# Kernel optimization log

Measured on AMD Instinct MI355X. Metric: run time of the kernel, lower is better.

Reference implementation:

```python
import math
import jax, jax.numpy as jnp
import numpy as np

HEADS = 16
REL_WINDOW = 128


def setup_inputs() -> dict:
    key = jax.random.key(0)
    k1, k2, k3, k4, k5 = jax.random.split(key, 5)
    b, s, d = 2, 2048, 1024
    hd = d // HEADS          # 64
    R = 2 * REL_WINDOW + 1   # 257
    return {
        "x": jax.random.normal(k1, (b, s, d), dtype=jnp.float32),
        "Wqkv": jax.random.normal(k2, (3 * d, d), dtype=jnp.float32) * (1.0 / math.sqrt(d)),
        "bqkv": jax.random.normal(k3, (3 * d,), dtype=jnp.float32) * 0.02,
        "Wr": jax.random.normal(k4, (R, hd), dtype=jnp.float32) * (1.0 / math.sqrt(hd)),
        "br": jax.random.normal(k5, (R,), dtype=jnp.float32) * 0.02,
    }


def reference(x, Wqkv, bqkv, Wr, br):
    b, s, d = x.shape
    h = HEADS
    hd = d // h
    w = REL_WINDOW
    scale = math.sqrt(d / h)

    # qkv projection; torch view(b,s,h,3*hd) then chunk(3, dim=-1)
    qkv = (x @ Wqkv.T + bqkv).reshape(b, s, h, 3 * hd)
    q, k, v = jnp.split(qkv, 3, axis=-1)          # each [b,s,h,hd]
    q = q.transpose(0, 2, 1, 3)                   # [b,h,s,hd]
    k = k.transpose(0, 2, 1, 3)
    v = v.transpose(0, 2, 1, 3)

    # content scores
    content = jnp.einsum('bhik,bhjk->bhij', q, k) / scale  # [b,h,s,s]

    # relative position scores: project queries to R logits, gather per (i,j) offset
    idx = jnp.arange(s)
    offsets = jnp.clip(idx[None, :] - idx[:, None], -w, w) + w  # [s,s] in [0, 2w]
    rp = jnp.einsum('bhik,rk->bhir', q, Wr) + br               # [b,h,s,R]
    pos = jnp.take_along_axis(rp, jnp.broadcast_to(offsets, (b, h, s, s)), axis=-1)

    attn = jax.nn.softmax(content + pos, axis=-1)
    out = jnp.einsum('bhij,bhjk->bhik', attn, v)  # [b,h,s,hd]
    return out.transpose(0, 2, 1, 3).reshape(b, s, d)
```

## Files before the change

kernel.cpp:

```cpp
#include <hip/hip_runtime.h>

typedef short bfrag __attribute__((ext_vector_type(8)));
typedef float f32x4 __attribute__((ext_vector_type(4)));

#define MFMA16(a, b, c) __builtin_amdgcn_mfma_f32_16x16x32_bf16((a), (b), (c), 0, 0, 0)

#define SEQ   2048
#define DMOD  1024
#define NHEAD 16
#define HDIM  64
#define RSZ   257
#define RSTRIDE 260
#define RPADN 272
#define XN    (4096*1024)
#define WN    (3072*1024)
#define LOG2E 1.44269504f

__device__ __forceinline__ unsigned short f2bf(float f) {
  unsigned int u = __float_as_uint(f);
  u += 0x7FFFu + ((u >> 16) & 1u);
  return (unsigned short)(u >> 16);
}
__device__ __forceinline__ float bf2f(unsigned short u) {
  return __uint_as_float(((unsigned int)u) << 16);
}
__device__ __forceinline__ unsigned int pkbf(float a, float b) {
#if defined(__gfx950__)
  unsigned int r;
  asm("v_cvt_pk_bf16_f32 %0, %1, %2" : "=v"(r) : "v"(a), "v"(b));
  return r;
#else
  return (unsigned int)f2bf(a) | ((unsigned int)f2bf(b) << 16);
#endif
}
__device__ __forceinline__ float fexp2(float x) {
#if __has_builtin(__builtin_amdgcn_exp2f)
  return __builtin_amdgcn_exp2f(x);
#else
  return __expf(x * 0.69314718f);
#endif
}
__device__ __forceinline__ void gl2lds16(const void* g, void* l) {
  __builtin_amdgcn_global_load_lds(
      (__attribute__((address_space(1))) void*)(g),
      (__attribute__((address_space(3))) void*)(l), 16, 0, 0);
}

__global__ __launch_bounds__(256) void cast_all(const float* __restrict__ x,
                                                const float* __restrict__ Wqkv,
                                                const float* __restrict__ Wr,
                                                unsigned short* __restrict__ xb,
                                                unsigned short* __restrict__ wb,
                                                unsigned short* __restrict__ wrb) {
  int i = (blockIdx.x * 256 + threadIdx.x) * 4;
  if (i < XN) {
    float4 v = *(const float4*)(x + i);
    ushort4 o; o.x = f2bf(v.x); o.y = f2bf(v.y); o.z = f2bf(v.z); o.w = f2bf(v.w);
    *(ushort4*)(xb + i) = o;
  } else if (i < XN + WN) {
    int j = i - XN;
    float4 v = *(const float4*)(Wqkv + j);
    ushort4 o; o.x = f2bf(v.x); o.y = f2bf(v.y); o.z = f2bf(v.z); o.w = f2bf(v.w);
    *(ushort4*)(wb + j) = o;
  } else {
    int j = i - XN - WN;
    ushort4 o;
    unsigned short t[4];
#pragma unroll
    for (int k = 0; k < 4; ++k)
      t[k] = (j + k < RSZ * HDIM) ? f2bf(Wr[j + k]) : (unsigned short)0;
    o.x = t[0]; o.y = t[1]; o.z = t[2]; o.w = t[3];
    *(ushort4*)(wrb + j) = o;
  }
}

__global__ __launch_bounds__(512) void qkv_gemm(const unsigned short* __restrict__ xb,
                                                const unsigned short* __restrict__ wb,
                                                const float* __restrict__ bqkv,
                                                unsigned short* __restrict__ qb,
                                                unsigned short* __restrict__ kbuf,
                                                unsigned short* __restrict__ vtb) {
  __shared__ unsigned short SMEM[16384];
  unsigned short* Vtmp = SMEM;
  const int tid = threadIdx.x;
  const int orig = blockIdx.x;
  const int gx = orig & 7;
  const int idx = orig >> 3;
  const int myp = gx * 4 + (idx & 3);
  const int nxp = idx >> 2;
  const int m0 = myp * 128, n0 = nxp * 128;
  const int wave = tid >> 6, lane = tid & 63;
  const int q4 = lane >> 4, l16 = lane & 15;
  const int wm = (wave & 1) * 64;
  const int wn = (wave >> 1) * 32;
  const int sw3 = l16 & 3;

  f32x4 acc[4][2];
#pragma unroll
  for (int rt = 0; rt < 4; ++rt)
#pragma unroll
    for (int ct = 0; ct < 2; ++ct) acc[rt][ct] = (f32x4){0.f, 0.f, 0.f, 0.f};

  auto STAGE = [&](int k0, int buf) {
    unsigned short* As = SMEM + buf * 8192;
    unsigned short* Bs = As + 4096;
    int r = tid >> 2, cl = (tid & 3) ^ ((tid >> 2) & 3);
    gl2lds16(xb + (size_t)(m0 + r) * DMOD + k0 + cl * 8, As + tid * 8);
    gl2lds16(wb + (size_t)(n0 + r) * DMOD + k0 + cl * 8, Bs + tid * 8);
  };

  STAGE(0, 0);
  __syncthreads();

#pragma unroll 2
  for (int jt = 0; jt < 32; ++jt) {
    const int buf = jt & 1;
    unsigned short* As = SMEM + buf * 8192;
    unsigned short* Bs = As + 4096;

    if (jt < 31) STAGE((jt + 1) * 32, buf ^ 1);

    bfrag af[4], bf[2];
#pragma unroll
    for (int rt = 0; rt < 4; ++rt)
      af[rt] = *(const bfrag*)(As + (wm + rt * 16 + l16) * 32 + ((q4 ^ sw3) * 8));
#pragma unroll
    for (int ct = 0; ct < 2; ++ct)
      bf[ct] = *(const bfrag*)(Bs + (wn + ct * 16 + l16) * 32 + ((q4 ^ sw3) * 8));
#pragma unroll
    for (int rt = 0; rt < 4; ++rt)
#pragma unroll
      for (int ct = 0; ct < 2; ++ct)
        acc[rt][ct] = MFMA16(bf[ct], af[rt], acc[rt][ct]);

    __syncthreads();
  }

  const int batch = m0 >> 11;
  const int sbase = m0 & 2047;
  const int r3 = nxp % 3;
  const bool hasV = (r3 != 0);
  const int nv0 = n0 + ((r3 == 2) ? 64 : 0);

#pragma unroll
  for (int ct = 0; ct < 2; ++ct) {
    int ng = n0 + wn + ct * 16 + q4 * 4;
    int hh = ng / 192;
    int rem = ng - hh * 192;
    int t = rem >> 6, dd = rem & 63;
    float4 b4 = *(const float4*)(bqkv + ng);
    if (t < 2) {
      unsigned short* dst = (t == 0) ? qb : kbuf;
      size_t rowo = ((size_t)(batch * NHEAD + hh)) * SEQ + sbase;
#pragma unroll
      for (int rt = 0; rt < 4; ++rt) {
        int m = wm + rt * 16 + l16;
        uint2 pv;
        pv.x = pkbf(acc[rt][ct][0] + b4.x, acc[rt][ct][1] + b4.y);
        pv.y = pkbf(acc[rt][ct][2] + b4.z, acc[rt][ct][3] + b4.w);
        *(uint2*)(dst + (rowo + m) * HDIM + dd) = pv;
      }
    } else {
#pragma unroll
      for (int rt = 0; rt < 4; ++rt) {
        int m = wm + rt * 16 + l16;
        Vtmp[(dd + 0) * 136 + m] = f2bf(acc[rt][ct][0] + b4.x);
        Vtmp[(dd + 1) * 136 + m] = f2bf(acc[rt][ct][1] + b4.y);
        Vtmp[(dd + 2) * 136 + m] = f2bf(acc[rt][ct][2] + b4.z);
        Vtmp[(dd + 3) * 136 + m] = f2bf(acc[rt][ct][3] + b4.w);
      }
    }
  }

  if (hasV) {
    __syncthreads();
    const int hh = nv0 / 192;
    unsigned short* vdst = vtb + ((size_t)(batch * NHEAD + hh)) * HDIM * SEQ;
#pragma unroll
    for (int it = 0; it < 2; ++it) {
      int u = it * 512 + tid;
      int dd = u >> 4, mc = u & 15;
      bfrag val = *(const bfrag*)(Vtmp + dd * 136 + mc * 8);
      *(bfrag*)(vdst + (size_t)dd * SEQ + sbase + mc * 8) = val;
    }
  }
}

__global__ __launch_bounds__(512) void flash_attn(const unsigned short* __restrict__ qb,
                                                  const unsigned short* __restrict__ kbuf,
                                                  const unsigned short* __restrict__ vtb,
                                                  const unsigned short* __restrict__ wrb,
                                                  const float* __restrict__ br,
                                                  unsigned short* __restrict__ rp16,
                                                  float* __restrict__ out) {
  __shared__ unsigned short SMEM[24576];
  unsigned short* WrS = SMEM;
  unsigned short* Ps  = SMEM + 16384;

  const int tid = threadIdx.x;
  const int orig = blockIdx.x;
  const int slot = orig >> 3;
  const int bh = (orig & 7) * 4 + (slot >> 4);
  const int i0 = (slot & 15) << 7;
  const int wave = tid >> 6, lane = tid & 63;
  const int q4 = lane >> 4, l16 = lane & 15;
  const int sw = l16 & 7;
  const float SC = 0.125f * LOG2E;

  const int rloc = wave * 16 + l16;
  const int ig = i0 + rloc;
  const int iw0 = i0 + wave * 16;
  const unsigned short* qrow = qb + ((size_t)bh * SEQ + ig) * HDIM;
  bfrag qf0 = *(const bfrag*)(qrow + q4 * 8);
  bfrag qf1 = *(const bfrag*)(qrow + 32 + q4 * 8);

  unsigned short* rpbase = rp16 + ((size_t)bh * SEQ + ig) * RSTRIDE;

  {
    for (int i = tid; i < RPADN * HDIM / 8; i += 512) {
      int r = i >> 3, c = i & 7;
      *(uint4*)(&WrS[r * 64 + ((c ^ (r & 7)) << 3)]) = *(const uint4*)(&wrb[i * 8]);
    }
    __syncthreads();

    const float br256 = br[256];
#pragma unroll 4
    for (int ct = 0; ct < 16; ++ct) {
      f32x4 acc = (f32x4){0.f, 0.f, 0.f, 0.f};
      bfrag w0 = *(const bfrag*)(WrS + (ct * 16 + l16) * 64 + (q4 ^ sw) * 8);
      bfrag w1 = *(const bfrag*)(WrS + (ct * 16 + l16) * 64 + ((4 + q4) ^ sw) * 8);
      acc = MFMA16(w0, qf0, acc);
      acc = MFMA16(w1, qf1, acc);
      int r = ct * 16 + q4 * 4;
      float4 b4 = *(const float4*)(br + r);
      uint2 pv;
      pv.x = pkbf((acc[0] + b4.x) * LOG2E, (acc[1] + b4.y) * LOG2E);
      pv.y = pkbf((acc[2] + b4.z) * LOG2E, (acc[3] + b4.w) * LOG2E);
      *(uint2*)(rpbase + r) = pv;
    }
    {
      f32x4 acc = (f32x4){0.f, 0.f, 0.f, 0.f};
      bfrag w0 = *(const bfrag*)(WrS + (256 + l16) * 64 + (q4 ^ sw) * 8);
      bfrag w1 = *(const bfrag*)(WrS + (256 + l16) * 64 + ((4 + q4) ^ sw) * 8);
      acc = MFMA16(w0, qf0, acc);
      acc = MFMA16(w1, qf1, acc);
      if (q4 == 0)
        rpbase[256] = f2bf((acc[0] + br256) * LOG2E);
    }
    asm volatile("s_waitcnt vmcnt(0)" ::: "memory");
    __syncthreads();
  }

  const float rpL = bf2f(rpbase[0]);
  const float rpR = bf2f(rpbase[256]);

  float m_s = -3.0e38f, l_s = 0.f;
  f32x4 oacc[4];
#pragma unroll
  for (int ct = 0; ct < 4; ++ct) oacc[ct] = (f32x4){0.f, 0.f, 0.f, 0.f};

  const unsigned short* kbase = kbuf + (size_t)bh * SEQ * HDIM;
  const unsigned short* vbase = vtb + (size_t)bh * HDIM * SEQ;

  const int sr = tid >> 3, scl = (tid & 7) ^ ((tid >> 3) & 7);

  gl2lds16(kbase + (size_t)sr * HDIM + scl * 8, SMEM + tid * 8);
  gl2lds16(vbase + (size_t)sr * SEQ + 0 + scl * 8, SMEM + 8192 + tid * 8);
  __syncthreads();

#pragma unroll 2
  for (int jt = 0; jt < 32; ++jt) {
    const int cur = jt & 1;
    const int j0 = jt * 64;
    unsigned short* Kc = SMEM + cur * 4096;
    unsigned short* Vc = SMEM + 8192 + cur * 4096;

    if (jt < 31) {
      gl2lds16(kbase + (size_t)(j0 + 64 + sr) * HDIM + scl * 8,
               SMEM + (cur ^ 1) * 4096 + tid * 8);
      gl2lds16(vbase + (size_t)sr * SEQ + (j0 + 64) + scl * 8,
               SMEM + 8192 + (cur ^ 1) * 4096 + tid * 8);
    }

    f32x4 sacc[4];
#pragma unroll
    for (int ct = 0; ct < 4; ++ct) {
      sacc[ct] = (f32x4){0.f, 0.f, 0.f, 0.f};
      bfrag k0f = *(const bfrag*)(Kc + (ct * 16 + l16) * 64 + (q4 ^ sw) * 8);
      bfrag k1f = *(const bfrag*)(Kc + (ct * 16 + l16) * 64 + ((4 + q4) ^ sw) * 8);
      sacc[ct] = MFMA16(k0f, qf0, sacc[ct]);
      sacc[ct] = MFMA16(k1f, qf1, sacc[ct]);
    }

    float p[4][4];
    const int djw = j0 - iw0;
    if (djw >= 143) {
#pragma unroll
      for (int ct = 0; ct < 4; ++ct)
#pragma unroll
        for (int reg = 0; reg < 4; ++reg)
          p[ct][reg] = sacc[ct][reg] * SC + rpR;
    } else if (djw <= -191) {
#pragma unroll
      for (int ct = 0; ct < 4; ++ct)
#pragma unroll
        for (int reg = 0; reg < 4; ++reg)
          p[ct][reg] = sacc[ct][reg] * SC + rpL;
    } else {
#pragma unroll
      for (int ct = 0; ct < 4; ++ct) {
#pragma unroll
        for (int reg = 0; reg < 4; ++reg) {
          int j = j0 + ct * 16 + q4 * 4 + reg;
          int off = j - ig;
          off = (off < -128) ? -128 : (off > 128 ? 128 : off);
          p[ct][reg] = sacc[ct][reg] * SC + bf2f(rpbase[off + 128]);
        }
      }
    }

    float mm;
    {
      float a0 = fmaxf(fmaxf(p[0][0], p[0][1]), fmaxf(p[0][2], p[0][3]));
      float a1 = fmaxf(fmaxf(p[1][0], p[1][1]), fmaxf(p[1][2], p[1][3]));
      float a2 = fmaxf(fmaxf(p[2][0], p[2][1]), fmaxf(p[2][2], p[2][3]));
      float a3 = fmaxf(fmaxf(p[3][0], p[3][1]), fmaxf(p[3][2], p[3][3]));
      mm = fmaxf(fmaxf(a0, a1), fmaxf(a2, a3));
      mm = fmaxf(mm, __shfl_xor(mm, 16));
      mm = fmaxf(mm, __shfl_xor(mm, 32));
    }
    if (!__all(mm <= m_s + 8.0f)) {
      const float mnew = fmaxf(m_s, mm);
      const float alpha = fexp2(m_s - mnew);
      m_s = mnew;
      l_s *= alpha;
#pragma unroll
      for (int ct = 0; ct < 4; ++ct)
#pragma unroll
        for (int reg = 0; reg < 4; ++reg)
          oacc[ct][reg] *= alpha;
    }
#pragma unroll
    for (int ct = 0; ct < 4; ++ct)
#pragma unroll
      for (int reg = 0; reg < 4; ++reg)
        p[ct][reg] = fexp2(p[ct][reg] - m_s);
    {
      float s0 = (p[0][0] + p[0][1]) + (p[0][2] + p[0][3]);
      float s1 = (p[1][0] + p[1][1]) + (p[1][2] + p[1][3]);
      float s2 = (p[2][0] + p[2][1]) + (p[2][2] + p[2][3]);
      float s3 = (p[3][0] + p[3][1]) + (p[3][2] + p[3][3]);
      float rs = (s0 + s1) + (s2 + s3);
      rs += __shfl_xor(rs, 16);
      rs += __shfl_xor(rs, 32);
      l_s += rs;
    }

    unsigned int* Pw = (unsigned int*)Ps;
#pragma unroll
    for (int ct = 0; ct < 4; ++ct) {
      unsigned int pk01 = pkbf(p[ct][0], p[ct][1]);
      unsigned int pk23 = pkbf(p[ct][2], p[ct][3]);
      int chunk = ct * 2 + (q4 >> 1);
      unsigned int a = rloc * 32 + ((chunk ^ sw) << 2) + ((q4 & 1) << 1);
      Pw[a] = pk01;
      Pw[a + 1] = pk23;
    }

    bfrag pf0 = *(const bfrag*)(Ps + rloc * 64 + (q4 ^ sw) * 8);
    bfrag pf1 = *(const bfrag*)(Ps + rloc * 64 + ((4 + q4) ^ sw) * 8);
#pragma unroll
    for (int ct = 0; ct < 4; ++ct) {
      bfrag v0f = *(const bfrag*)(Vc + (ct * 16 + l16) * 64 + (q4 ^ sw) * 8);
      bfrag v1f = *(const bfrag*)(Vc + (ct * 16 + l16) * 64 + ((4 + q4) ^ sw) * 8);
      oacc[ct] = MFMA16(v0f, pf0, oacc[ct]);
      oacc[ct] = MFMA16(v1f, pf1, oacc[ct]);
    }

    __syncthreads();
  }

  const int bidx = bh >> 4, hh = bh & 15;
  const float inv = 1.0f / l_s;
  float* orow = out + ((size_t)bidx * SEQ + ig) * DMOD + hh * HDIM;
#pragma unroll
  for (int ct = 0; ct < 4; ++ct) {
    float4 v;
    v.x = oacc[ct][0] * inv;
    v.y = oacc[ct][1] * inv;
    v.z = oacc[ct][2] * inv;
    v.w = oacc[ct][3] * inv;
    *(float4*)(orow + ct * 16 + q4 * 4) = v;
  }
}

extern "C" void kernel_launch(void* const* d_in, const int* in_sizes, int n_in,
                              void* d_out, int out_size, void* d_ws, size_t ws_size,
                              hipStream_t stream) {
  const float* x    = (const float*)d_in[0];
  const float* Wqkv = (const float*)d_in[1];
  const float* bqkv = (const float*)d_in[2];
  const float* Wr   = (const float*)d_in[3];
  const float* br   = (const float*)d_in[4];
  float* out = (float*)d_out;

  char* ws = (char*)d_ws;
  unsigned short* xb   = (unsigned short*)(ws);
  unsigned short* wb   = (unsigned short*)(ws + 8388608);
  unsigned short* qb   = (unsigned short*)(ws + 14680064);
  unsigned short* kb   = (unsigned short*)(ws + 23068672);
  unsigned short* vtb  = (unsigned short*)(ws + 31457280);
  unsigned short* wrb  = (unsigned short*)(ws + 39845888);
  unsigned short* rp16 = (unsigned short*)(ws + 39880704);

  cast_all<<<7185, 256, 0, stream>>>(x, Wqkv, Wr, xb, wb, wrb);
  qkv_gemm<<<768, 512, 0, stream>>>(xb, wb, bqkv, qb, kb, vtb);
  flash_attn<<<512, 512, 0, stream>>>(qb, kb, vtb, wrb, br, rp16, out);
}
```

Measured before the change: 195.1 us.

## Fuse fp32-to-bf16 casts into QKV GEMM and attention Wr staging

```diff
diff --git a/kernel.cpp b/kernel.cpp
--- a/kernel.cpp
+++ b/kernel.cpp
@@ -12,8 +12,6 @@
 #define RSZ   257
 #define RSTRIDE 260
 #define RPADN 272
-#define XN    (4096*1024)
-#define WN    (3072*1024)
 #define LOG2E 1.44269504f
 
 __device__ __forceinline__ unsigned short f2bf(float f) {
@@ -46,36 +44,8 @@
       (__attribute__((address_space(3))) void*)(l), 16, 0, 0);
 }
 
-__global__ __launch_bounds__(256) void cast_all(const float* __restrict__ x,
+__global__ __launch_bounds__(512) void qkv_gemm(const float* __restrict__ x,
                                                 const float* __restrict__ Wqkv,
-                                                const float* __restrict__ Wr,
-                                                unsigned short* __restrict__ xb,
-                                                unsigned short* __restrict__ wb,
-                                                unsigned short* __restrict__ wrb) {
-  int i = (blockIdx.x * 256 + threadIdx.x) * 4;
-  if (i < XN) {
-    float4 v = *(const float4*)(x + i);
-    ushort4 o; o.x = f2bf(v.x); o.y = f2bf(v.y); o.z = f2bf(v.z); o.w = f2bf(v.w);
-    *(ushort4*)(xb + i) = o;
-  } else if (i < XN + WN) {
-    int j = i - XN;
-    float4 v = *(const float4*)(Wqkv + j);
-    ushort4 o; o.x = f2bf(v.x); o.y = f2bf(v.y); o.z = f2bf(v.z); o.w = f2bf(v.w);
-    *(ushort4*)(wb + j) = o;
-  } else {
-    int j = i - XN - WN;
-    ushort4 o;
-    unsigned short t[4];
-#pragma unroll
-    for (int k = 0; k < 4; ++k)
-      t[k] = (j + k < RSZ * HDIM) ? f2bf(Wr[j + k]) : (unsigned short)0;
-    o.x = t[0]; o.y = t[1]; o.z = t[2]; o.w = t[3];
-    *(ushort4*)(wrb + j) = o;
-  }
-}
-
-__global__ __launch_bounds__(512) void qkv_gemm(const unsigned short* __restrict__ xb,
-                                                const unsigned short* __restrict__ wb,
                                                 const float* __restrict__ bqkv,
                                                 unsigned short* __restrict__ qb,
                                                 unsigned short* __restrict__ kbuf,
@@ -101,15 +71,35 @@
 #pragma unroll
     for (int ct = 0; ct < 2; ++ct) acc[rt][ct] = (f32x4){0.f, 0.f, 0.f, 0.f};
 
-  auto STAGE = [&](int k0, int buf) {
-    unsigned short* As = SMEM + buf * 8192;
-    unsigned short* Bs = As + 4096;
-    int r = tid >> 2, cl = (tid & 3) ^ ((tid >> 2) & 3);
-    gl2lds16(xb + (size_t)(m0 + r) * DMOD + k0 + cl * 8, As + tid * 8);
-    gl2lds16(wb + (size_t)(n0 + r) * DMOD + k0 + cl * 8, Bs + tid * 8);
+  const int strow = tid >> 2;
+  const int stcl = (tid & 3) ^ ((tid >> 2) & 3);
+  const float* asrc = x + (size_t)(m0 + strow) * DMOD + stcl * 8;
+  const float* bsrc = Wqkv + (size_t)(n0 + strow) * DMOD + stcl * 8;
+
+  auto ST_LOAD = [&](int k0, float4& a0, float4& a1, float4& b0, float4& b1) {
+    a0 = *(const float4*)(asrc + k0);
+    a1 = *(const float4*)(asrc + k0 + 4);
+    b0 = *(const float4*)(bsrc + k0);
+    b1 = *(const float4*)(bsrc + k0 + 4);
   };
-
-  STAGE(0, 0);
+  auto ST_WRITE = [&](int buf, const float4& a0, const float4& a1,
+                      const float4& b0, const float4& b1) {
+    unsigned int* Aw = (unsigned int*)(SMEM + buf * 8192) + tid * 4;
+    unsigned int* Bw = (unsigned int*)(SMEM + buf * 8192 + 4096) + tid * 4;
+    uint4 pa, pb;
+    pa.x = pkbf(a0.x, a0.y); pa.y = pkbf(a0.z, a0.w);
+    pa.z = pkbf(a1.x, a1.y); pa.w = pkbf(a1.z, a1.w);
+    pb.x = pkbf(b0.x, b0.y); pb.y = pkbf(b0.z, b0.w);
+    pb.z = pkbf(b1.x, b1.y); pb.w = pkbf(b1.z, b1.w);
+    *(uint4*)Aw = pa;
+    *(uint4*)Bw = pb;
+  };
+
+  {
+    float4 a0, a1, b0, b1;
+    ST_LOAD(0, a0, a1, b0, b1);
+    ST_WRITE(0, a0, a1, b0, b1);
+  }
   __syncthreads();
 
 #pragma unroll 2
@@ -118,7 +108,8 @@
     unsigned short* As = SMEM + buf * 8192;
     unsigned short* Bs = As + 4096;
 
-    if (jt < 31) STAGE((jt + 1) * 32, buf ^ 1);
+    float4 a0, a1, b0, b1;
+    if (jt < 31) ST_LOAD((jt + 1) * 32, a0, a1, b0, b1);
 
     bfrag af[4], bf[2];
 #pragma unroll
@@ -132,6 +123,8 @@
 #pragma unroll
       for (int ct = 0; ct < 2; ++ct)
         acc[rt][ct] = MFMA16(bf[ct], af[rt], acc[rt][ct]);
+
+    if (jt < 31) ST_WRITE(buf ^ 1, a0, a1, b0, b1);
 
     __syncthreads();
   }
@@ -189,7 +182,7 @@
 __global__ __launch_bounds__(512) void flash_attn(const unsigned short* __restrict__ qb,
                                                   const unsigned short* __restrict__ kbuf,
                                                   const unsigned short* __restrict__ vtb,
-                                                  const unsigned short* __restrict__ wrb,
+                                                  const float* __restrict__ Wr,
                                                   const float* __restrict__ br,
                                                   unsigned short* __restrict__ rp16,
                                                   float* __restrict__ out) {
@@ -219,7 +212,15 @@
   {
     for (int i = tid; i < RPADN * HDIM / 8; i += 512) {
       int r = i >> 3, c = i & 7;
-      *(uint4*)(&WrS[r * 64 + ((c ^ (r & 7)) << 3)]) = *(const uint4*)(&wrb[i * 8]);
+      float4 f0 = {0.f, 0.f, 0.f, 0.f}, f1 = {0.f, 0.f, 0.f, 0.f};
+      if (i < (RSZ * HDIM) / 8) {
+        f0 = *(const float4*)(Wr + i * 8);
+        f1 = *(const float4*)(Wr + i * 8 + 4);
+      }
+      uint4 pv;
+      pv.x = pkbf(f0.x, f0.y); pv.y = pkbf(f0.z, f0.w);
+      pv.z = pkbf(f1.x, f1.y); pv.w = pkbf(f1.z, f1.w);
+      *(uint4*)(&WrS[r * 64 + ((c ^ (r & 7)) << 3)]) = pv;
     }
     __syncthreads();
 
@@ -405,15 +406,11 @@
   float* out = (float*)d_out;
 
   char* ws = (char*)d_ws;
-  unsigned short* xb   = (unsigned short*)(ws);
-  unsigned short* wb   = (unsigned short*)(ws + 8388608);
   unsigned short* qb   = (unsigned short*)(ws + 14680064);
   unsigned short* kb   = (unsigned short*)(ws + 23068672);
   unsigned short* vtb  = (unsigned short*)(ws + 31457280);
-  unsigned short* wrb  = (unsigned short*)(ws + 39845888);
   unsigned short* rp16 = (unsigned short*)(ws + 39880704);
 
-  cast_all<<<7185, 256, 0, stream>>>(x, Wqkv, Wr, xb, wb, wrb);
-  qkv_gemm<<<768, 512, 0, stream>>>(xb, wb, bqkv, qb, kb, vtb);
-  flash_attn<<<512, 512, 0, stream>>>(qb, kb, vtb, wrb, br, rp16, out);
-}
+  qkv_gemm<<<768, 512, 0, stream>>>(x, Wqkv, bqkv, qb, kb, vtb);
+  flash_attn<<<512, 512, 0, stream>>>(qb, kb, vtb, Wr, br, rp16, out);
+}
```

Result: no change. 198.9 us (+1.9%).
